# Kernel optimization log

Measured on AMD Instinct MI355X. Metric: run time of the kernel, lower is better.

## Reference

```python
import jax, jax.numpy as jnp
import numpy as np

NUM_USER = 60000
NUM_ITEM = 40000
DIM_C = 64
NUM_EDGES = 1_000_000
NUM_ROUTING = 3
ALPHA_THRESHOLD = 0.02
REATTN = True
NEG_SLOPE = 0.2  # PyG GAT default leaky-relu slope
EPS = 1e-16


def l2norm(x):
    # F.normalize(x): L2 along last dim with eps clamp
    return x / jnp.clip(jnp.linalg.norm(x, axis=-1, keepdims=True), 1e-12, None)


def seg_softmax(s, seg, n):
    # numerically stable softmax over edges grouped by target node
    m = jax.ops.segment_max(s, seg, num_segments=n)
    e = jnp.exp(s - m[seg])
    den = jax.ops.segment_sum(e, seg, num_segments=n)
    return e / (den[seg] + EPS)


def setup_inputs() -> dict:
    key = jax.random.key(0)
    ks = jax.random.split(key, 6)
    xav = (2.0 / (NUM_USER + DIM_C)) ** 0.5  # xavier_normal_ scale for preference
    features = jax.random.normal(ks[0], (NUM_ITEM, DIM_C), jnp.float32)
    features2 = jax.random.normal(ks[1], (NUM_ITEM, DIM_C), jnp.float32)
    features3 = jax.random.normal(ks[2], (NUM_ITEM, DIM_C), jnp.float32)
    preference = jax.random.normal(ks[3], (NUM_USER, DIM_C), jnp.float32) * xav
    users = jax.random.randint(ks[4], (NUM_EDGES,), 0, NUM_USER, dtype=jnp.int32)
    items = jax.random.randint(ks[5], (NUM_EDGES,), 0, NUM_ITEM, dtype=jnp.int32) + NUM_USER
    edge_index = jnp.stack([users, items], axis=0)  # [2, E] user -> item (item ids offset by num_user)
    return {"features": features, "features2": features2, "features3": features3,
            "preference": preference, "edge_index": edge_index}


def reference(features, features2, features3, preference, edge_index):
    n = NUM_USER + NUM_ITEM
    inv_sqrt_d = 1.0 / np.sqrt(DIM_C).astype(np.float32)

    pref = l2norm(preference)
    x = jnp.concatenate([pref, l2norm(features)], axis=0)   # [N, d]
    y = jnp.concatenate([pref, l2norm(features2)], axis=0)
    z = jnp.concatenate([pref, l2norm(features3)], axis=0)

    # symmetrize: edge_index = cat(edge_index, edge_index[[1,0]])
    ei = jnp.concatenate([edge_index, edge_index[::-1]], axis=1)  # [2, 2E]
    src, dst = ei[0], ei[1]  # message flows src(j) -> dst(i)

    # --- conv_embed_1: multimodal GAT with thresholding + re-attention ---
    s = ((x[dst] * x[src]).sum(-1)
         + (y[dst] * y[src]).sum(-1)
         + (z[dst] * z[src]).sum(-1)) * inv_sqrt_d          # [2E]
    alpha = seg_softmax(jax.nn.leaky_relu(s, NEG_SLOPE), dst, n)
    alpha_t = jnp.where(alpha > ALPHA_THRESHOLD, alpha, 0.0)
    if REATTN:
        den = jax.ops.segment_sum(alpha_t, dst, num_segments=n)
        alpha_t = alpha_t / (den[dst] + EPS)
    x_hat = jax.ops.segment_sum(x[src] * alpha_t[:, None], dst, num_segments=n)
    x = l2norm(x + x_hat)

    # --- routing iterations with plain dot-product GAT (conv_embed_2) ---
    for _ in range(NUM_ROUTING):
        s2 = (x[dst] * x[src]).sum(-1) * inv_sqrt_d
        a2 = seg_softmax(jax.nn.leaky_relu(s2, NEG_SLOPE), dst, n)
        x_hat = jax.ops.segment_sum(x[src] * a2[:, None], dst, num_segments=n)
        x = l2norm(x + x_hat)

    return x, alpha_t.reshape(-1, 1)
```

## Files before the change

kernel.cpp:

```cpp
#include <hip/hip_runtime.h>

#define NU 60000
#define NI 40000
#define NN 100000
#define NE 1000000
#define NE2 2000000
#define DC 64

#define M_CONV1 0.375f
#define M_ROUTE 0.125f

typedef unsigned short u16;

__device__ __forceinline__ float grp16_sum(float v) {
    v += __shfl_xor(v, 1, 64);
    v += __shfl_xor(v, 2, 64);
    v += __shfl_xor(v, 4, 64);
    v += __shfl_xor(v, 8, 64);
    return v;
}
__device__ __forceinline__ float xgrp_sum(float v) {
    v += __shfl_xor(v, 16, 64);
    v += __shfl_xor(v, 32, 64);
    return v;
}
__device__ __forceinline__ float4 xgrp_sum4(float4 v) {
    v.x = xgrp_sum(v.x); v.y = xgrp_sum(v.y); v.z = xgrp_sum(v.z); v.w = xgrp_sum(v.w);
    return v;
}
__device__ __forceinline__ float dot4(float4 a, float4 b) {
    return a.x * b.x + a.y * b.y + a.z * b.z + a.w * b.w;
}
__device__ __forceinline__ u16 f2b(float f) {
    union { float f; unsigned u; } a; a.f = f;
    unsigned r = a.u + 0x7FFFu + ((a.u >> 16) & 1u);
    return (u16)(r >> 16);
}
__device__ __forceinline__ float b2f(u16 b) {
    union { unsigned u; float f; } a; a.u = ((unsigned)b) << 16;
    return a.f;
}
__device__ __forceinline__ float4 b2f4(ushort4 h) {
    float4 f; f.x = b2f(h.x); f.y = b2f(h.y); f.z = b2f(h.z); f.w = b2f(h.w);
    return f;
}

__global__ __launch_bounds__(256) void k_init(const float* __restrict__ f1,
                                              const float* __restrict__ f2,
                                              const float* __restrict__ f3,
                                              const float* __restrict__ pref,
                                              float* __restrict__ x0,
                                              u16* __restrict__ x016,
                                              float* __restrict__ w) {
    int node = (blockIdx.x * blockDim.x + threadIdx.x) >> 6;
    int lane = threadIdx.x & 63;
    if (node >= NN) return;
    float outv;
    if (node < NU) {
        float v = pref[node * DC + lane];
        float s = v * v;
#pragma unroll
        for (int o = 32; o > 0; o >>= 1) s += __shfl_xor(s, o, 64);
        outv = v / fmaxf(sqrtf(s), 1e-12f);
    } else {
        int it = node - NU;
        float a = f1[it * DC + lane];
        float b = f2[it * DC + lane];
        float c = f3[it * DC + lane];
        float sa = a * a, sb = b * b, sc = c * c;
#pragma unroll
        for (int o = 32; o > 0; o >>= 1) {
            sa += __shfl_xor(sa, o, 64);
            sb += __shfl_xor(sb, o, 64);
            sc += __shfl_xor(sc, o, 64);
        }
        outv = a / fmaxf(sqrtf(sa), 1e-12f);
        w[it * DC + lane] = outv + b / fmaxf(sqrtf(sb), 1e-12f) + c / fmaxf(sqrtf(sc), 1e-12f);
    }
    x0[node * DC + lane] = outv;
    x016[node * DC + lane] = f2b(outv);
}

__global__ __launch_bounds__(256) void k_count(const int* __restrict__ ei,
                                               int* __restrict__ cnt) {
    int e = blockIdx.x * blockDim.x + threadIdx.x;
    if (e >= NE2) return;
    int dst = (e < NE) ? ei[NE + e] : ei[e - NE];
    atomicAdd(&cnt[dst], 1);
}

__device__ __forceinline__ int block_exscan1024(int v) {
    __shared__ int wsum[16];
    int tid = threadIdx.x, lane = tid & 63;
    int wv = tid >> 6;
    int inc = v;
#pragma unroll
    for (int o = 1; o < 64; o <<= 1) {
        int t = __shfl_up(inc, o, 64);
        if (lane >= o) inc += t;
    }
    if (lane == 63) wsum[wv] = inc;
    __syncthreads();
    if (tid < 16) {
        int b = wsum[tid];
        int binc = b;
#pragma unroll
        for (int o = 1; o < 16; o <<= 1) {
            int t = __shfl_up(binc, o, 16);
            if (tid >= o) binc += t;
        }
        wsum[tid] = binc - b;
    }
    __syncthreads();
    return wsum[wv] + inc - v;
}

__global__ __launch_bounds__(1024) void k_scan1(const int* __restrict__ cnt,
                                                int* __restrict__ off,
                                                int* __restrict__ bsum) {
    int i = blockIdx.x * 1024 + threadIdx.x;
    int v = (i < NN) ? cnt[i] : 0;
    int ex = block_exscan1024(v);
    if (i < NN) off[i] = ex;
    if (threadIdx.x == 1023) bsum[blockIdx.x] = ex + v;
}

__global__ __launch_bounds__(1024) void k_scan2(int* __restrict__ bsum, int nb) {
    int v = (threadIdx.x < nb) ? bsum[threadIdx.x] : 0;
    int ex = block_exscan1024(v);
    if (threadIdx.x < nb) bsum[threadIdx.x] = ex;
}

__global__ __launch_bounds__(1024) void k_scan3(int* __restrict__ off,
                                                const int* __restrict__ bsum,
                                                int* __restrict__ cur) {
    int i = blockIdx.x * 1024 + threadIdx.x;
    if (i < NN) {
        int o = off[i] + bsum[blockIdx.x];
        off[i] = o;
        cur[i] = o;
    }
    if (i == 0) off[NN] = NE2;
}

__global__ __launch_bounds__(256) void k_fill(const int* __restrict__ ei,
                                              int* __restrict__ cur,
                                              int* __restrict__ eid,
                                              int* __restrict__ esrc) {
    int e = blockIdx.x * blockDim.x + threadIdx.x;
    if (e >= NE2) return;
    int src = ei[e];
    int dst = (e < NE) ? ei[NE + e] : ei[e - NE];
    int pos = atomicAdd(&cur[dst], 1);
    eid[pos] = e;
    esrc[pos] = src;
}

__global__ __launch_bounds__(256) void k_conv1(const float* __restrict__ x0,
                                               const float* __restrict__ w,
                                               const u16* __restrict__ x16,
                                               const int* __restrict__ off,
                                               const int* __restrict__ eid,
                                               const int* __restrict__ esrc,
                                               float* __restrict__ sE,
                                               float* __restrict__ x1,
                                               u16* __restrict__ x116,
                                               float* __restrict__ aout) {
    int node = (blockIdx.x * blockDim.x + threadIdx.x) >> 6;
    int lane = threadIdx.x & 63;
    if (node >= NN) return;
    int grp = lane >> 4, gl = lane & 15;
    int beg = off[node], end = off[node + 1];
    bool user = (node < NU);

    float4 xi4 = *((const float4*)(x0 + (size_t)node * DC) + gl);
    float4 ai4 = user ? xi4 : *((const float4*)(w + (size_t)(node - NU) * DC) + gl);
    const float* gbase = user ? w : x0;
    int goff = user ? NU : 0;

    float den = 0.f;
    for (int p0 = beg; p0 < end; p0 += 8) {
        int pA = p0 + grp, pB = p0 + 4 + grp;
        bool aA = pA < end, aB = pB < end;
        int sA = aA ? (esrc[pA] - goff) : 0;
        int sB = aB ? (esrc[pB] - goff) : 0;
        float4 gA = *((const float4*)(gbase + (size_t)sA * DC) + gl);
        float4 gB = *((const float4*)(gbase + (size_t)sB * DC) + gl);
        float dA = grp16_sum(dot4(ai4, gA)) * 0.125f;
        float dB = grp16_sum(dot4(ai4, gB)) * 0.125f;
        dA = (dA > 0.f) ? dA : 0.2f * dA;
        dB = (dB > 0.f) ? dB : 0.2f * dB;
        float eA = aA ? __expf(dA - M_CONV1) : 0.f;
        float eB = aB ? __expf(dB - M_CONV1) : 0.f;
        den += eA + eB;
        if (aA && gl == 0) sE[pA] = eA;
        if (aB && gl == 0) sE[pB] = eB;
    }
    den = xgrp_sum(den);
    float invden = 1.f / (den + 1e-16f);
    asm volatile("s_waitcnt vmcnt(0)" ::: "memory");

    float den2 = 0.f;
    float4 xh = {0.f, 0.f, 0.f, 0.f};
    for (int p0 = beg; p0 < end; p0 += 8) {
        int pA = p0 + grp, pB = p0 + 4 + grp;
        bool aA = pA < end, aB = pB < end;
        int sA = aA ? esrc[pA] : 0;
        int sB = aB ? esrc[pB] : 0;
        ushort4 hA = *((const ushort4*)(x16 + (size_t)sA * DC) + gl);
        ushort4 hB = *((const ushort4*)(x16 + (size_t)sB * DC) + gl);
        float eA = aA ? sE[pA] : 0.f;
        float eB = aB ? sE[pB] : 0.f;
        float aAv = eA * invden, aBv = eB * invden;
        float tA = (aAv > 0.02f) ? aAv : 0.f;
        float tB = (aBv > 0.02f) ? aBv : 0.f;
        den2 += tA + tB;
        float4 fA = b2f4(hA);
        float4 fB = b2f4(hB);
        xh.x += tA * fA.x + tB * fB.x;
        xh.y += tA * fA.y + tB * fB.y;
        xh.z += tA * fA.z + tB * fB.z;
        xh.w += tA * fA.w + tB * fB.w;
    }
    den2 = xgrp_sum(den2);
    xh = xgrp_sum4(xh);
    float invden2 = 1.f / (den2 + 1e-16f);

    for (int p = beg + lane; p < end; p += 64) {
        float a = sE[p] * invden;
        float t = (a > 0.02f) ? a : 0.f;
        aout[eid[p]] = t * invden2;
    }

    float4 v;
    v.x = xi4.x + xh.x * invden2;
    v.y = xi4.y + xh.y * invden2;
    v.z = xi4.z + xh.z * invden2;
    v.w = xi4.w + xh.w * invden2;
    float nn = grp16_sum(dot4(v, v));
    float inv_n = 1.f / fmaxf(sqrtf(nn), 1e-12f);
    if (grp == 0) {
        float4 o = {v.x * inv_n, v.y * inv_n, v.z * inv_n, v.w * inv_n};
        *((float4*)(x1 + (size_t)node * DC) + gl) = o;
        ushort4 h = {f2b(o.x), f2b(o.y), f2b(o.z), f2b(o.w)};
        *((ushort4*)(x116 + (size_t)node * DC) + gl) = h;
    }
}

__global__ __launch_bounds__(256) void k_route(const float* __restrict__ xin,
                                               const u16* __restrict__ g16,
                                               const int* __restrict__ off,
                                               const int* __restrict__ esrc,
                                               float* __restrict__ xout,
                                               u16* __restrict__ out16) {
    int node = (blockIdx.x * blockDim.x + threadIdx.x) >> 6;
    int lane = threadIdx.x & 63;
    if (node >= NN) return;
    int grp = lane >> 4, gl = lane & 15;
    int beg = off[node], end = off[node + 1];

    float4 xi4 = *((const float4*)(xin + (size_t)node * DC) + gl);

    float den = 0.f;
    float4 xh = {0.f, 0.f, 0.f, 0.f};
    for (int p0 = beg; p0 < end; p0 += 8) {
        int pA = p0 + grp, pB = p0 + 4 + grp;
        bool aA = pA < end, aB = pB < end;
        int sA = aA ? esrc[pA] : 0;
        int sB = aB ? esrc[pB] : 0;
        ushort4 hA = *((const ushort4*)(g16 + (size_t)sA * DC) + gl);
        ushort4 hB = *((const ushort4*)(g16 + (size_t)sB * DC) + gl);
        float4 fA = b2f4(hA);
        float4 fB = b2f4(hB);
        float dA = grp16_sum(dot4(xi4, fA)) * 0.125f;
        float dB = grp16_sum(dot4(xi4, fB)) * 0.125f;
        dA = (dA > 0.f) ? dA : 0.2f * dA;
        dB = (dB > 0.f) ? dB : 0.2f * dB;
        float eA = aA ? __expf(dA - M_ROUTE) : 0.f;
        float eB = aB ? __expf(dB - M_ROUTE) : 0.f;
        den += eA + eB;
        xh.x += eA * fA.x + eB * fB.x;
        xh.y += eA * fA.y + eB * fB.y;
        xh.z += eA * fA.z + eB * fB.z;
        xh.w += eA * fA.w + eB * fB.w;
    }
    den = xgrp_sum(den);
    xh = xgrp_sum4(xh);
    float inv = 1.f / (den + 1e-16f);

    float4 v;
    v.x = xi4.x + xh.x * inv;
    v.y = xi4.y + xh.y * inv;
    v.z = xi4.z + xh.z * inv;
    v.w = xi4.w + xh.w * inv;
    float nn = grp16_sum(dot4(v, v));
    float inv_n = 1.f / fmaxf(sqrtf(nn), 1e-12f);
    if (grp == 0) {
        float4 o = {v.x * inv_n, v.y * inv_n, v.z * inv_n, v.w * inv_n};
        *((float4*)(xout + (size_t)node * DC) + gl) = o;
        ushort4 h = {f2b(o.x), f2b(o.y), f2b(o.z), f2b(o.w)};
        *((ushort4*)(out16 + (size_t)node * DC) + gl) = h;
    }
}

extern "C" void kernel_launch(void* const* d_in, const int* in_sizes, int n_in,
                              void* d_out, int out_size, void* d_ws, size_t ws_size,
                              hipStream_t stream) {
    const float* f1   = (const float*)d_in[0];
    const float* f2   = (const float*)d_in[1];
    const float* f3   = (const float*)d_in[2];
    const float* pref = (const float*)d_in[3];
    const int*   ei   = (const int*)d_in[4];

    float* out  = (float*)d_out;
    float* x0   = out;
    float* aout = out + (size_t)NN * DC;

    float* xb   = (float*)d_ws;
    float* w    = xb + (size_t)NN * DC;
    float* sE   = w + (size_t)NI * DC;
    u16*  xa16  = (u16*)(sE + NE2);
    u16*  xb16  = xa16 + (size_t)NN * DC;
    int* cnt    = (int*)(xb16 + (size_t)NN * DC);
    int* off    = cnt + NN;
    int* bsum   = off + NN + 1;
    int* eid    = bsum + 1024;
    int* esrc   = eid + NE2;

    hipMemsetAsync(cnt, 0, NN * sizeof(int), stream);

    int nb = (NN + 1023) / 1024;
    k_init<<<(NN * 64) / 256, 256, 0, stream>>>(f1, f2, f3, pref, x0, xa16, w);
    k_count<<<(NE2 + 255) / 256, 256, 0, stream>>>(ei, cnt);
    k_scan1<<<nb, 1024, 0, stream>>>(cnt, off, bsum);
    k_scan2<<<1, 1024, 0, stream>>>(bsum, nb);
    k_scan3<<<nb, 1024, 0, stream>>>(off, bsum, cnt);
    k_fill<<<(NE2 + 255) / 256, 256, 0, stream>>>(ei, cnt, eid, esrc);

    k_conv1<<<(NN * 64) / 256, 256, 0, stream>>>(x0, w, xa16, off, eid, esrc, sE, xb, xb16, aout);
    k_route<<<(NN * 64) / 256, 256, 0, stream>>>(xb, xb16, off, esrc, x0, xa16);
    k_route<<<(NN * 64) / 256, 256, 0, stream>>>(x0, xa16, off, esrc, xb, xb16);
    k_route<<<(NN * 64) / 256, 256, 0, stream>>>(xb, xb16, off, esrc, x0, xa16);
}
```

Measured before the change: 636.0 us.

## Two-pass binned CSR build and batched neighbor index loads in gather loops

Replaces the single scattered atomic fill of the CSR with two passes. Edges are first binned into 25-node buckets with one global atomic per edge, then each block places its bucket's edges using shared-memory atomics, which should give more local writes and less global atomic contention. The gather loops in conv1 and route now load 16 neighbor indices (and attention values) with one coalesced load, broadcast them by shuffle, and issue four independent row gathers per iteration to raise memory-level parallelism. The binned buffer aliases the sE workspace, and edge ids are packed as e<<5, which fits within int range for 2M edges.

```diff
diff --git a/kernel.cpp b/kernel.cpp
--- a/kernel.cpp
+++ b/kernel.cpp
@@ -6,6 +6,9 @@
 #define NE 1000000
 #define NE2 2000000
 #define DC 64
+
+#define KPB 25
+#define NB 4000
 
 #define M_CONV1 0.375f
 #define M_ROUTE 0.125f
@@ -133,27 +136,47 @@
 
 __global__ __launch_bounds__(1024) void k_scan3(int* __restrict__ off,
                                                 const int* __restrict__ bsum,
-                                                int* __restrict__ cur) {
+                                                int* __restrict__ bcur) {
     int i = blockIdx.x * 1024 + threadIdx.x;
     if (i < NN) {
         int o = off[i] + bsum[blockIdx.x];
         off[i] = o;
-        cur[i] = o;
+        if (i % KPB == 0) bcur[i / KPB] = o;
     }
     if (i == 0) off[NN] = NE2;
 }
 
-__global__ __launch_bounds__(256) void k_fill(const int* __restrict__ ei,
-                                              int* __restrict__ cur,
-                                              int* __restrict__ eid,
-                                              int* __restrict__ esrc) {
+__global__ __launch_bounds__(256) void k_bin(const int* __restrict__ ei,
+                                             int* __restrict__ bcur,
+                                             int2* __restrict__ binned) {
     int e = blockIdx.x * blockDim.x + threadIdx.x;
     if (e >= NE2) return;
     int src = ei[e];
     int dst = (e < NE) ? ei[NE + e] : ei[e - NE];
-    int pos = atomicAdd(&cur[dst], 1);
-    eid[pos] = e;
-    esrc[pos] = src;
+    int b = dst / KPB;
+    int drel = dst - b * KPB;
+    int pos = atomicAdd(&bcur[b], 1);
+    int2 v; v.x = src; v.y = (e << 5) | drel;
+    binned[pos] = v;
+}
+
+__global__ __launch_bounds__(128) void k_fill2(const int2* __restrict__ binned,
+                                               const int* __restrict__ off,
+                                               int* __restrict__ esrcF,
+                                               int* __restrict__ eidF) {
+    int b = blockIdx.x;
+    __shared__ int cur[KPB];
+    int t = threadIdx.x;
+    if (t < KPB) cur[t] = off[b * KPB + t];
+    __syncthreads();
+    int s = off[b * KPB], e = off[b * KPB + KPB];
+    for (int p = s + t; p < e; p += 128) {
+        int2 v = binned[p];
+        int drel = v.y & 31;
+        int pos = atomicAdd(&cur[drel], 1);
+        esrcF[pos] = v.x;
+        eidF[pos] = v.y >> 5;
+    }
 }
 
 __global__ __launch_bounds__(256) void k_conv1(const float* __restrict__ x0,
@@ -179,22 +202,25 @@
     int goff = user ? NU : 0;
 
     float den = 0.f;
-    for (int p0 = beg; p0 < end; p0 += 8) {
-        int pA = p0 + grp, pB = p0 + 4 + grp;
-        bool aA = pA < end, aB = pB < end;
-        int sA = aA ? (esrc[pA] - goff) : 0;
-        int sB = aB ? (esrc[pB] - goff) : 0;
-        float4 gA = *((const float4*)(gbase + (size_t)sA * DC) + gl);
-        float4 gB = *((const float4*)(gbase + (size_t)sB * DC) + gl);
-        float dA = grp16_sum(dot4(ai4, gA)) * 0.125f;
-        float dB = grp16_sum(dot4(ai4, gB)) * 0.125f;
-        dA = (dA > 0.f) ? dA : 0.2f * dA;
-        dB = (dB > 0.f) ? dB : 0.2f * dB;
-        float eA = aA ? __expf(dA - M_CONV1) : 0.f;
-        float eB = aB ? __expf(dB - M_CONV1) : 0.f;
-        den += eA + eB;
-        if (aA && gl == 0) sE[pA] = eA;
-        if (aB && gl == 0) sE[pB] = eB;
+    for (int p0 = beg; p0 < end; p0 += 16) {
+        int pl = p0 + lane;
+        int eidx = (lane < 16 && pl < end) ? (esrc[pl] - goff) : 0;
+        int s0[4]; float4 g[4];
+#pragma unroll
+        for (int c = 0; c < 4; ++c) {
+            s0[c] = __shfl(eidx, 4 * c + grp, 64);
+            g[c] = *((const float4*)(gbase + (size_t)s0[c] * DC) + gl);
+        }
+#pragma unroll
+        for (int c = 0; c < 4; ++c) {
+            int p = p0 + 4 * c + grp;
+            bool act = p < end;
+            float d = grp16_sum(dot4(ai4, g[c])) * 0.125f;
+            d = (d > 0.f) ? d : 0.2f * d;
+            float e = act ? __expf(d - M_CONV1) : 0.f;
+            den += e;
+            if (act && gl == 0) sE[p] = e;
+        }
     }
     den = xgrp_sum(den);
     float invden = 1.f / (den + 1e-16f);
@@ -202,25 +228,26 @@
 
     float den2 = 0.f;
     float4 xh = {0.f, 0.f, 0.f, 0.f};
-    for (int p0 = beg; p0 < end; p0 += 8) {
-        int pA = p0 + grp, pB = p0 + 4 + grp;
-        bool aA = pA < end, aB = pB < end;
-        int sA = aA ? esrc[pA] : 0;
-        int sB = aB ? esrc[pB] : 0;
-        ushort4 hA = *((const ushort4*)(x16 + (size_t)sA * DC) + gl);
-        ushort4 hB = *((const ushort4*)(x16 + (size_t)sB * DC) + gl);
-        float eA = aA ? sE[pA] : 0.f;
-        float eB = aB ? sE[pB] : 0.f;
-        float aAv = eA * invden, aBv = eB * invden;
-        float tA = (aAv > 0.02f) ? aAv : 0.f;
-        float tB = (aBv > 0.02f) ? aBv : 0.f;
-        den2 += tA + tB;
-        float4 fA = b2f4(hA);
-        float4 fB = b2f4(hB);
-        xh.x += tA * fA.x + tB * fB.x;
-        xh.y += tA * fA.y + tB * fB.y;
-        xh.z += tA * fA.z + tB * fB.z;
-        xh.w += tA * fA.w + tB * fB.w;
+    for (int p0 = beg; p0 < end; p0 += 16) {
+        int pl = p0 + lane;
+        bool ldok = (lane < 16 && pl < end);
+        int eidx = ldok ? esrc[pl] : 0;
+        float sv = ldok ? sE[pl] : 0.f;
+        int s0[4]; ushort4 h[4];
+#pragma unroll
+        for (int c = 0; c < 4; ++c) {
+            s0[c] = __shfl(eidx, 4 * c + grp, 64);
+            h[c] = *((const ushort4*)(x16 + (size_t)s0[c] * DC) + gl);
+        }
+#pragma unroll
+        for (int c = 0; c < 4; ++c) {
+            float e = __shfl(sv, 4 * c + grp, 64);
+            float a = e * invden;
+            float t = (a > 0.02f) ? a : 0.f;
+            den2 += t;
+            float4 f = b2f4(h[c]);
+            xh.x += t * f.x; xh.y += t * f.y; xh.z += t * f.z; xh.w += t * f.w;
+        }
     }
     den2 = xgrp_sum(den2);
     xh = xgrp_sum4(xh);
@@ -263,26 +290,25 @@
 
     float den = 0.f;
     float4 xh = {0.f, 0.f, 0.f, 0.f};
-    for (int p0 = beg; p0 < end; p0 += 8) {
-        int pA = p0 + grp, pB = p0 + 4 + grp;
-        bool aA = pA < end, aB = pB < end;
-        int sA = aA ? esrc[pA] : 0;
-        int sB = aB ? esrc[pB] : 0;
-        ushort4 hA = *((const ushort4*)(g16 + (size_t)sA * DC) + gl);
-        ushort4 hB = *((const ushort4*)(g16 + (size_t)sB * DC) + gl);
-        float4 fA = b2f4(hA);
-        float4 fB = b2f4(hB);
-        float dA = grp16_sum(dot4(xi4, fA)) * 0.125f;
-        float dB = grp16_sum(dot4(xi4, fB)) * 0.125f;
-        dA = (dA > 0.f) ? dA : 0.2f * dA;
-        dB = (dB > 0.f) ? dB : 0.2f * dB;
-        float eA = aA ? __expf(dA - M_ROUTE) : 0.f;
-        float eB = aB ? __expf(dB - M_ROUTE) : 0.f;
-        den += eA + eB;
-        xh.x += eA * fA.x + eB * fB.x;
-        xh.y += eA * fA.y + eB * fB.y;
-        xh.z += eA * fA.z + eB * fB.z;
-        xh.w += eA * fA.w + eB * fB.w;
+    for (int p0 = beg; p0 < end; p0 += 16) {
+        int pl = p0 + lane;
+        int eidx = (lane < 16 && pl < end) ? esrc[pl] : 0;
+        int s0[4]; ushort4 h[4];
+#pragma unroll
+        for (int c = 0; c < 4; ++c) {
+            s0[c] = __shfl(eidx, 4 * c + grp, 64);
+            h[c] = *((const ushort4*)(g16 + (size_t)s0[c] * DC) + gl);
+        }
+#pragma unroll
+        for (int c = 0; c < 4; ++c) {
+            bool act = (p0 + 4 * c + grp) < end;
+            float4 f = b2f4(h[c]);
+            float d = grp16_sum(dot4(xi4, f)) * 0.125f;
+            d = (d > 0.f) ? d : 0.2f * d;
+            float e = act ? __expf(d - M_ROUTE) : 0.f;
+            den += e;
+            xh.x += e * f.x; xh.y += e * f.y; xh.z += e * f.z; xh.w += e * f.w;
+        }
     }
     den = xgrp_sum(den);
     xh = xgrp_sum4(xh);
@@ -318,13 +344,15 @@
 
     float* xb   = (float*)d_ws;
     float* w    = xb + (size_t)NN * DC;
-    float* sE   = w + (size_t)NI * DC;
-    u16*  xa16  = (u16*)(sE + NE2);
+    int2*  binned = (int2*)(w + (size_t)NI * DC);
+    float* sE   = (float*)binned;
+    u16*  xa16  = (u16*)(binned + NE2);
     u16*  xb16  = xa16 + (size_t)NN * DC;
     int* cnt    = (int*)(xb16 + (size_t)NN * DC);
     int* off    = cnt + NN;
     int* bsum   = off + NN + 1;
-    int* eid    = bsum + 1024;
+    int* bcur   = bsum + 1024;
+    int* eid    = bcur + NB;
     int* esrc   = eid + NE2;
 
     hipMemsetAsync(cnt, 0, NN * sizeof(int), stream);
@@ -334,8 +362,9 @@
     k_count<<<(NE2 + 255) / 256, 256, 0, stream>>>(ei, cnt);
     k_scan1<<<nb, 1024, 0, stream>>>(cnt, off, bsum);
     k_scan2<<<1, 1024, 0, stream>>>(bsum, nb);
-    k_scan3<<<nb, 1024, 0, stream>>>(off, bsum, cnt);
-    k_fill<<<(NE2 + 255) / 256, 256, 0, stream>>>(ei, cnt, eid, esrc);
+    k_scan3<<<nb, 1024, 0, stream>>>(off, bsum, bcur);
+    k_bin<<<(NE2 + 255) / 256, 256, 0, stream>>>(ei, bcur, binned);
+    k_fill2<<<NB, 128, 0, stream>>>(binned, off, esrc, eid);
 
     k_conv1<<<(NN * 64) / 256, 256, 0, stream>>>(x0, w, xa16, off, eid, esrc, sE, xb, xb16, aout);
     k_route<<<(NN * 64) / 256, 256, 0, stream>>>(xb, xb16, off, esrc, x0, xa16);
```

Result: slower. 681.7 us (+7.2%).
